# Kernel tuning notes

Measured on AMD Instinct MI355X. Metric: run time of the kernel, lower is better.

Reference implementation:

```python
import jax, jax.numpy as jnp
import numpy as np


def setup_inputs() -> dict:
    key = jax.random.key(0)
    k1, k2, k3, k4 = jax.random.split(key, 4)
    B, S, H, D = 4, 2048, 1024, 1024
    X = jax.random.normal(k1, (B, S, H), dtype=jnp.float32)
    # nn.Linear weight stored as [out, in]; we store as [in, out] for x @ W
    scale = 1.0 / np.sqrt(H)
    Wq = jax.random.normal(k2, (H, D), dtype=jnp.float32) * scale
    Wk = jax.random.normal(k3, (H, D), dtype=jnp.float32) * scale
    Wv = jax.random.normal(k4, (H, D), dtype=jnp.float32) * scale
    return {"X": X, "Wq": Wq, "Wk": Wk, "Wv": Wv}


def reference(X, Wq, Wk, Wv):
    B, S, H = X.shape
    q = X @ Wq  # [B, S, D]
    k = X @ Wk
    v = X @ Wv
    D = k.shape[-1]
    scores = jnp.einsum('bqd,bkd->bqk', q, k) / jnp.sqrt(jnp.float32(D))
    causal = jnp.tril(jnp.ones((S, S), dtype=bool))  # block_size mask sliced to S
    scores = jnp.where(causal, scores, -jnp.inf)
    weights = jax.nn.softmax(scores, axis=-1)  # dropout p=0.0 -> identity
    return jnp.einsum('bqk,bkd->bqd', weights, v)
```

## Files before the change

### kernel.cpp

```cpp
#include <hip/hip_runtime.h>

#define AS1 __attribute__((address_space(1)))
#define AS3 __attribute__((address_space(3)))

typedef __attribute__((ext_vector_type(8))) short short8;
typedef __attribute__((ext_vector_type(4))) float floatx4;

__device__ __forceinline__ short f2bf(float f) {
  union { float f; unsigned u; } v; v.f = f;
  return (short)((v.u + 0x7fffu + ((v.u >> 16) & 1u)) >> 16);
}
__device__ __forceinline__ float bf2f(short s) {
  union { unsigned u; float f; } v; v.u = ((unsigned)(unsigned short)s) << 16;
  return v.f;
}

__device__ __forceinline__ void gload_lds16(const void* g, void* l) {
  __builtin_amdgcn_global_load_lds((const AS1 unsigned*)g, (AS3 unsigned*)l, 16, 0, 0);
}

__device__ __forceinline__ void stage128x64(const short* __restrict__ G, long rowBase, long ld,
                                            int kBase, short* lds, int lane, int wave) {
  const int chunk = (lane & 7) ^ ((lane >> 3) & 7);
  const short* gb = G + rowBase * ld + (long)kBase + (long)(lane >> 3) * ld + chunk * 8;
#pragma unroll
  for (int j = 0; j < 4; ++j) {
    int c = wave * 4 + j;
    gload_lds16(gb + (long)c * 8 * ld, lds + c * 512);
  }
}

__device__ __forceinline__ void mfma_step(const short* lA, const short* lB, floatx4 acc[4][4],
                                          int lane, int wm, int wn) {
#pragma unroll
  for (int kk = 0; kk < 64; kk += 32) {
    short8 a[4], b[4];
    int kq = (kk + (lane >> 4) * 8) ^ ((lane & 7) << 3);
#pragma unroll
    for (int i = 0; i < 4; ++i) {
      a[i] = *(const short8*)(lA + (wm * 64 + i * 16 + (lane & 15)) * 64 + kq);
      b[i] = *(const short8*)(lB + (wn * 64 + i * 16 + (lane & 15)) * 64 + kq);
    }
#pragma unroll
    for (int i = 0; i < 4; ++i)
#pragma unroll
      for (int j = 0; j < 4; ++j)
        acc[i][j] = __builtin_amdgcn_mfma_f32_16x16x32_bf16(a[i], b[j], acc[i][j], 0, 0, 0);
  }
}

__device__ const unsigned char PAIR_LUT[136] = {
  0x40,0x41,0x42,0x43,0x50,0x51,0x52,0x53,0x60,0x61,0x62,0x63,0x70,0x71,0x72,0x73,
  0x80,0x81,0x82,0x83,0x90,0x91,0x92,0x93,0xA0,0xA1,0xA2,0xA3,0xB0,0xB1,0xB2,0xB3,
  0x84,0x85,0x86,0x87,0x94,0x95,0x96,0x97,0xA4,0xA5,0xA6,0xA7,0xB4,0xB5,0xB6,0xB7,
  0xC0,0xC1,0xC2,0xC3,0xD0,0xD1,0xD2,0xD3,0xE0,0xE1,0xE2,0xE3,0xF0,0xF1,0xF2,0xF3,
  0xC4,0xC5,0xC6,0xC7,0xD4,0xD5,0xD6,0xD7,0xE4,0xE5,0xE6,0xE7,0xF4,0xF5,0xF6,0xF7,
  0xC8,0xC9,0xCA,0xCB,0xD8,0xD9,0xDA,0xDB,0xE8,0xE9,0xEA,0xEB,0xF8,0xF9,0xFA,0xFB,
  0x00,0x10,0x11,0x20,0x21,0x22,0x30,0x31,0x32,0x33,
  0x44,0x54,0x55,0x64,0x65,0x66,0x74,0x75,0x76,0x77,
  0x88,0x98,0x99,0xA8,0xA9,0xAA,0xB8,0xB9,0xBA,0xBB,
  0xCC,0xDC,0xDD,0xEC,0xED,0xEE,0xFC,0xFD,0xFE,0xFF
};

__global__ void prep_inputs(const float* __restrict__ X, const float* __restrict__ Wq,
                            const float* __restrict__ Wk, const float* __restrict__ Wv,
                            short* __restrict__ Xb, short* __restrict__ Wt,
                            float* __restrict__ l) {
  __shared__ float t[32][33];
  if (blockIdx.x < 8192) {
    long i = ((long)blockIdx.x * 256 + threadIdx.x) * 4;
    float4 v = *(const float4*)(X + i);
    short4 o;
    o.x = f2bf(v.x); o.y = f2bf(v.y); o.z = f2bf(v.z); o.w = f2bf(v.w);
    *(short4*)(Xb + i) = o;
  } else if (blockIdx.x < 11264) {
    int idx = blockIdx.x - 8192;
    int z = idx >> 10, rem = idx & 1023;
    int bx = rem >> 5, by = rem & 31;
    const float* W = z == 0 ? Wq : (z == 1 ? Wk : Wv);
    short* O = Wt + (long)z * 1024 * 1024;
    int tx = threadIdx.x & 31, ty = threadIdx.x >> 5;
    int x = bx * 32 + tx;
    int y0 = by * 32;
    for (int j = ty; j < 32; j += 8)
      t[j][tx] = W[(long)(y0 + j) * 1024 + x];
    __syncthreads();
    int x2 = by * 32 + tx;
    int y2 = bx * 32;
    for (int j = ty; j < 32; j += 8)
      O[(long)(y2 + j) * 1024 + x2] = f2bf(t[tx][j]);
  } else {
    l[(blockIdx.x - 11264) * 256 + threadIdx.x] = 0.0f;
  }
}

#define LOFF(b, m, h) ((((b) * 2 + (m)) * 2 + (h)) * 8192)
#define MEMFENCE() asm volatile("" ::: "memory")
#define SBAR() do { MEMFENCE(); __builtin_amdgcn_s_barrier(); MEMFENCE(); } while (0)
#define SCHEDB() __builtin_amdgcn_sched_barrier(0)

__device__ __forceinline__ void stage_half(const short* __restrict__ g, short* l, int wv) {
  gload_lds16(g, l + wv * 512);
  gload_lds16(g + 65536, l + 4096 + wv * 512);
}

__device__ __forceinline__ short8 lds_rd(const short* l, int row, int kk, int lane) {
  const int r = row + (lane & 15);
  const int c = (kk + ((lane >> 4) << 3)) ^ ((lane & 7) << 3);
  return *(const short8*)(l + r * 64 + c);
}

__global__ __launch_bounds__(512, 2) void gemm_qkv(const short* __restrict__ Xb,
                                                   const short* __restrict__ Wt,
                                                   short* __restrict__ Q, short* __restrict__ K2,
                                                   short* __restrict__ Vt) {
  __shared__ __align__(16) short lds[65536];
  const int tid = threadIdx.x;
  const int lane = tid & 63, wv = tid >> 6;
  const int wm = wv >> 2, wn = wv & 3;

  const int bid = blockIdx.x;
  const int xcd = bid & 7, w = bid >> 3;
  const int mt = xcd * 4 + (w / 12);
  const int ng = w % 12;
  const int z = ng >> 2;
  const long mBase = (long)mt * 256;
  const long nBase = (long)(ng & 3) * 256;
  const short* Bm = Wt + (long)z * 1048576;

  const int r0 = tid >> 3;
  const int cc = ((tid & 7) ^ (r0 & 7)) << 3;
  const short* gA = Xb + (mBase + r0) * 1024 + cc;
  const short* gB = Bm + (nBase + r0) * 1024 + cc;

  floatx4 acc[8][4];
  const floatx4 zero = {0.f, 0.f, 0.f, 0.f};
#pragma unroll
  for (int i = 0; i < 8; ++i)
#pragma unroll
    for (int j = 0; j < 4; ++j) acc[i][j] = zero;

  short8 a0[4][2], a1[4][2], bq[2][2];

  stage_half(gA, lds + LOFF(0, 0, 0), wv);
  stage_half(gA + 131072, lds + LOFF(0, 0, 1), wv);
  stage_half(gB, lds + LOFF(0, 1, 0), wv);
  stage_half(gB + 131072, lds + LOFF(0, 1, 1), wv);
  stage_half(gA + 64, lds + LOFF(1, 0, 0), wv);
  stage_half(gA + 64 + 131072, lds + LOFF(1, 0, 1), wv);
  stage_half(gB + 64, lds + LOFF(1, 1, 0), wv);
  asm volatile("s_waitcnt vmcnt(6)" ::: "memory");
  SBAR();
  {
    const short* Ab0 = lds + LOFF(0, 0, wm);
#pragma unroll
    for (int f = 0; f < 4; ++f) a0[f][0] = lds_rd(Ab0, f * 16, 0, lane);
#pragma unroll
    for (int f = 0; f < 4; ++f) a0[f][1] = lds_rd(Ab0, f * 16, 32, lane);
  }

#pragma unroll 2
  for (int t = 0; t < 16; ++t) {
    const int buf = t & 1;
    const short* Ab  = lds + LOFF(buf, 0, wm);
    const short* Bb  = lds + LOFF(buf, 1, (wn >> 1));
    const short* AbN = lds + LOFF(buf ^ 1, 0, wm);
    const int brow = (wn & 1) * 64;

    bq[0][0] = lds_rd(Bb, brow, 0, lane);
    bq[1][0] = lds_rd(Bb, brow + 16, 0, lane);
    bq[0][1] = lds_rd(Bb, brow, 32, lane);
    bq[1][1] = lds_rd(Bb, brow + 16, 32, lane);
#pragma unroll
    for (int f = 0; f < 4; ++f) a1[f][0] = lds_rd(Ab, 64 + f * 16, 0, lane);
#pragma unroll
    for (int f = 0; f < 4; ++f) a1[f][1] = lds_rd(Ab, 64 + f * 16, 32, lane);
    if (t < 15) stage_half(gB + (t + 1) * 64 + 131072, lds + LOFF(buf ^ 1, 1, 1), wv);
    asm volatile("s_waitcnt lgkmcnt(8)" ::: "memory");
    SCHEDB();
    __builtin_amdgcn_s_setprio(1);
#pragma unroll
    for (int f = 0; f < 4; ++f)
#pragma unroll
      for (int n = 0; n < 2; ++n)
        acc[f][n] = __builtin_amdgcn_mfma_f32_16x16x32_bf16(a0[f][0], bq[n][0], acc[f][n], 0, 0, 0);
#pragma unroll
    for (int f = 0; f < 4; ++f)
#pragma unroll
      for (int n = 0; n < 2; ++n)
        acc[f][n] = __builtin_amdgcn_mfma_f32_16x16x32_bf16(a0[f][1], bq[n][1], acc[f][n], 0, 0, 0);
    __builtin_amdgcn_s_setprio(0);

    asm volatile("s_waitcnt lgkmcnt(0)" ::: "memory");
    SCHEDB();
    __builtin_amdgcn_s_setprio(1);
#pragma unroll
    for (int f = 0; f < 4; ++f)
#pragma unroll
      for (int n = 0; n < 2; ++n)
        acc[4 + f][n] = __builtin_amdgcn_mfma_f32_16x16x32_bf16(a1[f][0], bq[n][0], acc[4 + f][n], 0, 0, 0);
#pragma unroll
    for (int f = 0; f < 4; ++f)
#pragma unroll
      for (int n = 0; n < 2; ++n)
        acc[4 + f][n] = __builtin_amdgcn_mfma_f32_16x16x32_bf16(a1[f][1], bq[n][1], acc[4 + f][n], 0, 0, 0);
    __builtin_amdgcn_s_setprio(0);
    SBAR();

    bq[0][0] = lds_rd(Bb, brow + 32, 0, lane);
    bq[1][0] = lds_rd(Bb, brow + 48, 0, lane);
    bq[0][1] = lds_rd(Bb, brow + 32, 32, lane);
    bq[1][1] = lds_rd(Bb, brow + 48, 32, lane);
    if (t < 14) stage_half(gA + (t + 2) * 64, lds + LOFF(buf, 0, 0), wv);
    asm volatile("s_waitcnt lgkmcnt(0)" ::: "memory");
    SCHEDB();
    __builtin_amdgcn_s_setprio(1);
#pragma unroll
    for (int f = 0; f < 4; ++f)
#pragma unroll
      for (int n = 0; n < 2; ++n)
        acc[f][2 + n] = __builtin_amdgcn_mfma_f32_16x16x32_bf16(a0[f][0], bq[n][0], acc[f][2 + n], 0, 0, 0);
#pragma unroll
    for (int f = 0; f < 4; ++f)
#pragma unroll
      for (int n = 0; n < 2; ++n)
        acc[f][2 + n] = __builtin_amdgcn_mfma_f32_16x16x32_bf16(a0[f][1], bq[n][1], acc[f][2 + n], 0, 0, 0);
    __builtin_amdgcn_s_setprio(0);
    if (t < 14) { asm volatile("s_waitcnt vmcnt(2)" ::: "memory"); }
    else        { asm volatile("s_waitcnt vmcnt(0)" ::: "memory"); }
    SBAR();

    if (t < 15) {
#pragma unroll
      for (int f = 0; f < 4; ++f) a0[f][0] = lds_rd(AbN, f * 16, 0, lane);
#pragma unroll
      for (int f = 0; f < 4; ++f) a0[f][1] = lds_rd(AbN, f * 16, 32, lane);
    }
    if (t < 14) {
      stage_half(gA + (t + 2) * 64 + 131072, lds + LOFF(buf, 0, 1), wv);
      stage_half(gB + (t + 2) * 64, lds + LOFF(buf, 1, 0), wv);
    }
    SCHEDB();
    __builtin_amdgcn_s_setprio(1);
#pragma unroll
    for (int f = 0; f < 4; ++f)
#pragma unroll
      for (int n = 0; n < 2; ++n)
        acc[4 + f][2 + n] = __builtin_amdgcn_mfma_f32_16x16x32_bf16(a1[f][0], bq[n][0], acc[4 + f][2 + n], 0, 0, 0);
#pragma unroll
    for (int f = 0; f < 4; ++f)
#pragma unroll
      for (int n = 0; n < 2; ++n)
        acc[4 + f][2 + n] = __builtin_amdgcn_mfma_f32_16x16x32_bf16(a1[f][1], bq[n][1], acc[4 + f][2 + n], 0, 0, 0);
    __builtin_amdgcn_s_setprio(0);
  }

  if (z < 2) {
    short* outp = (z == 0) ? Q : K2;
#pragma unroll
    for (int f = 0; f < 8; ++f)
#pragma unroll
      for (int n = 0; n < 4; ++n) {
        const int col = (int)nBase + wn * 64 + n * 16 + (lane & 15);
#pragma unroll
        for (int rr = 0; rr < 4; ++rr) {
          const long m = mBase + wm * 128 + f * 16 + ((lane >> 4) << 2) + rr;
          outp[m * 1024 + col] = f2bf(acc[f][n][rr]);
        }
      }
  } else {
    const long bz = mBase >> 11;
    const int sB = (int)(mBase & 2047);
#pragma unroll
    for (int f = 0; f < 8; ++f) {
      const int s0 = sB + wm * 128 + f * 16 + ((lane >> 4) << 2);
#pragma unroll
      for (int n = 0; n < 4; ++n) {
        const int col = (int)nBase + wn * 64 + n * 16 + (lane & 15);
        short4 o;
        o.x = f2bf(acc[f][n][0]); o.y = f2bf(acc[f][n][1]);
        o.z = f2bf(acc[f][n][2]); o.w = f2bf(acc[f][n][3]);
        *(short4*)(Vt + ((bz * 1024 + col) * 2048 + s0)) = o;
      }
    }
  }
}

__global__ __launch_bounds__(256, 4) void scores_exp(const short* __restrict__ Q,
                                                     const short* __restrict__ Kk,
                                                     short* __restrict__ E, float* __restrict__ l) {
  __shared__ short lbuf[16384];
  short* lA = lbuf;
  short* lB = lbuf + 8192;
  const int lane = threadIdx.x & 63, wave = threadIdx.x >> 6;
  const int wm = wave >> 1, wn = wave & 1;
  const int b = blockIdx.y;

  const int r = blockIdx.x & 7, w = blockIdx.x >> 3;
  const int code = PAIR_LUT[r * 17 + w];
  const int qt = code >> 4, kt = code & 15;

  const long rowQ = (long)b * 2048 + (long)qt * 128;
  const long rowK = (long)b * 2048 + (long)kt * 128;

  floatx4 acc[4][4];
  const floatx4 zero = {0.f, 0.f, 0.f, 0.f};
#pragma unroll
  for (int i = 0; i < 4; ++i)
#pragma unroll
    for (int j = 0; j < 4; ++j) acc[i][j] = zero;

  for (int it = 0; it < 16; ++it) {
    stage128x64(Q, rowQ, 1024, it * 64, lA, lane, wave);
    stage128x64(Kk, rowK, 1024, it * 64, lB, lane, wave);
    __syncthreads();
    mfma_step(lA, lB, acc, lane, wm, wn);
    __syncthreads();
  }

  float* lrow = l + (long)b * 2048;
#pragma unroll
  for (int i = 0; i < 4; ++i) {
#pragma unroll
    for (int rr = 0; rr < 4; ++rr) {
      int ri = wm * 64 + i * 16 + (lane >> 4) * 4 + rr;
      int qrow = qt * 128 + ri;
      float psum = 0.f;
#pragma unroll
      for (int j = 0; j < 4; ++j) {
        int ci = wn * 64 + j * 16 + (lane & 15);
        int col = kt * 128 + ci;
        float sc = acc[i][j][rr] * 0.03125f;
        float e = (col <= qrow) ? __expf(sc) : 0.0f;
        short eb = f2bf(e);
        lbuf[ri * 128 + ((((ci >> 3) ^ (ri & 15)) << 3) | (ci & 7))] = eb;
        psum += bf2f(eb);
      }
      for (int m = 1; m < 16; m <<= 1) psum += __shfl_xor(psum, m, 64);
      if ((lane & 15) == 0) atomicAdd(&lrow[qrow], psum);
    }
  }
  __syncthreads();

  short* Eb = E + (long)b * 4194304;
  const long ebase = (long)(qt * 128) * 2048 + kt * 128;
#pragma unroll
  for (int pp = 0; pp < 8; ++pp) {
    int g = pp * 256 + threadIdx.x;
    int row = g >> 4, c = g & 15;
    short8 v = *(const short8*)(lbuf + row * 128 + ((c ^ (row & 15)) << 3));
    *(short8*)(Eb + ebase + (long)row * 2048 + c * 8) = v;
  }
}

__global__ __launch_bounds__(256, 4) void pv_gemm(const short* __restrict__ E,
                                                  const short* __restrict__ Vt,
                                                  const float* __restrict__ l,
                                                  float* __restrict__ part,
                                                  float* __restrict__ out) {
  __shared__ short lA[128 * 64], lB[128 * 64];
  const int lane = threadIdx.x & 63, wave = threadIdx.x >> 6;
  const int wm = wave >> 1, wn = wave & 1;
  const int xx = blockIdx.x;
  const int dt = xx / 24;
  const int within = xx % 24;
  const int r = within & 7, wsel = within >> 3;
  const int b = blockIdx.y;

  int qt, it0, it1, mode;
  if (wsel == 2) {
    qt = r; it0 = 0; it1 = (qt + 1) * 2; mode = 0;
  } else {
    qt = 15 - r;
    const int T = (qt + 1) * 2, c0 = T >> 1;
    if (wsel == 0) { it0 = 0;  it1 = c0; mode = 1; }
    else           { it0 = c0; it1 = T;  mode = 2; }
  }

  const short* Eb = E + (long)b * 2048 * 2048;
  const short* Vb = Vt + (long)b * 1024 * 2048;
  const float* lrow = l + (long)b * 2048;

  floatx4 acc[4][4];
  const floatx4 zero = {0.f, 0.f, 0.f, 0.f};
#pragma unroll
  for (int i = 0; i < 4; ++i)
#pragma unroll
    for (int j = 0; j < 4; ++j) acc[i][j] = zero;

  for (int it = it0; it < it1; ++it) {
    stage128x64(Eb, (long)qt * 128, 2048, it * 64, lA, lane, wave);
    stage128x64(Vb, (long)dt * 128, 2048, it * 64, lB, lane, wave);
    __syncthreads();
    mfma_step(lA, lB, acc, lane, wm, wn);
    __syncthreads();
  }

  if (mode == 2) {
    float* P = part + ((((long)b * 8 + (qt - 8)) * 8 + dt) << 14);
#pragma unroll
    for (int i = 0; i < 4; ++i)
#pragma unroll
      for (int rr = 0; rr < 4; ++rr) {
        int ri = wm * 64 + i * 16 + (lane >> 4) * 4 + rr;
#pragma unroll
        for (int j = 0; j < 4; ++j) {
          int ci = wn * 64 + j * 16 + (lane & 15);
          P[ri * 128 + ci] = acc[i][j][rr];
        }
      }
  } else {
#pragma unroll
    for (int i = 0; i < 4; ++i)
#pragma unroll
      for (int rr = 0; rr < 4; ++rr) {
        int qrow = qt * 128 + wm * 64 + i * 16 + (lane >> 4) * 4 + rr;
        float scale = (mode == 0) ? 1.0f / lrow[qrow] : 1.0f;
#pragma unroll
        for (int j = 0; j < 4; ++j) {
          int d = dt * 128 + wn * 64 + j * 16 + (lane & 15);
          out[((long)b * 2048 + qrow) * 1024 + d] = acc[i][j][rr] * scale;
        }
      }
  }
}

__global__ void pv_reduce(float* __restrict__ out, const float* __restrict__ part,
                          const float* __restrict__ l) {
  const int idx = blockIdx.x;
  const int b = idx >> 10;
  const int row = 1024 + (idx & 1023);
  const int t = threadIdx.x;
  const int dt = t >> 5, dl = (t << 2) & 127;
  const float inv = 1.0f / l[((long)b << 11) + row];
  const long pbase = ((((long)b * 8 + ((row >> 7) - 8)) * 8 + dt) << 14) + ((row & 127) << 7) + dl;
  const long obase = (((long)b * 2048 + row) << 10) + (t << 2);
  float4 o = *(const float4*)(out + obase);
  float4 p = *(const float4*)(part + pbase);
  o.x = (o.x + p.x) * inv; o.y = (o.y + p.y) * inv;
  o.z = (o.z + p.z) * inv; o.w = (o.w + p.w) * inv;
  *(float4*)(out + obase) = o;
}

extern "C" void kernel_launch(void* const* d_in, const int* in_sizes, int n_in,
                              void* d_out, int out_size, void* d_ws, size_t ws_size,
                              hipStream_t stream) {
  const float* X  = (const float*)d_in[0];
  const float* Wq = (const float*)d_in[1];
  const float* Wk = (const float*)d_in[2];
  const float* Wv = (const float*)d_in[3];

  char* ws = (char*)d_ws;
  short* Xb = (short*)(ws);
  short* Wt = (short*)(ws + 16777216L);
  short* Q  = (short*)(ws + 23068672L);
  short* K2 = (short*)(ws + 39845888L);
  short* Vt = (short*)(ws + 56623104L);
  short* E  = (short*)(ws + 73400320L);
  float* l  = (float*)(ws + 106954752L);
  float* part = (float*)(ws);

  prep_inputs<<<11296, 256, 0, stream>>>(X, Wq, Wk, Wv, Xb, Wt, l);
  gemm_qkv<<<384, 512, 0, stream>>>(Xb, Wt, Q, K2, Vt);
  scores_exp<<<dim3(136, 4), 256, 0, stream>>>(Q, K2, E, l);
  pv_gemm<<<dim3(192, 4), 256, 0, stream>>>(E, Vt, l, part, (float*)d_out);
  pv_reduce<<<4096, 256, 0, stream>>>((float*)d_out, part, l);
}
```

Baseline: 237.2 us.

## Double-buffer LDS staging in scores and PV GEMM kernels with async prefetch

Replaces the single-buffered load/sync/compute loops in scores_exp and pv_gemm with a two-stage LDS ring. The next K-tile is prefetched via global_load_lds while the current tile is consumed, with explicit vmcnt/lgkmcnt waits, sched barriers and setprio around the MFMA blocks. This aims to hide global memory latency behind the matrix math and to split LDS reads from MFMA issue. LDS per block doubles and launch bounds drop from 4 to 2 blocks per SM, which cuts occupancy.

```diff
diff --git a/kernel.cpp b/kernel.cpp
--- a/kernel.cpp
+++ b/kernel.cpp
@@ -30,24 +30,15 @@
   }
 }
 
-__device__ __forceinline__ void mfma_step(const short* lA, const short* lB, floatx4 acc[4][4],
-                                          int lane, int wm, int wn) {
-#pragma unroll
-  for (int kk = 0; kk < 64; kk += 32) {
-    short8 a[4], b[4];
-    int kq = (kk + (lane >> 4) * 8) ^ ((lane & 7) << 3);
-#pragma unroll
-    for (int i = 0; i < 4; ++i) {
-      a[i] = *(const short8*)(lA + (wm * 64 + i * 16 + (lane & 15)) * 64 + kq);
-      b[i] = *(const short8*)(lB + (wn * 64 + i * 16 + (lane & 15)) * 64 + kq);
-    }
-#pragma unroll
-    for (int i = 0; i < 4; ++i)
-#pragma unroll
-      for (int j = 0; j < 4; ++j)
-        acc[i][j] = __builtin_amdgcn_mfma_f32_16x16x32_bf16(a[i], b[j], acc[i][j], 0, 0, 0);
-  }
-}
+__device__ __forceinline__ short8 lds_rd(const short* l, int row, int kk, int lane) {
+  const int r = row + (lane & 15);
+  const int c = (kk + ((lane >> 4) << 3)) ^ ((lane & 7) << 3);
+  return *(const short8*)(l + r * 64 + c);
+}
+
+#define MEMFENCE() asm volatile("" ::: "memory")
+#define SBAR() do { MEMFENCE(); __builtin_amdgcn_s_barrier(); MEMFENCE(); } while (0)
+#define SCHEDB() __builtin_amdgcn_sched_barrier(0)
 
 __device__ const unsigned char PAIR_LUT[136] = {
   0x40,0x41,0x42,0x43,0x50,0x51,0x52,0x53,0x60,0x61,0x62,0x63,0x70,0x71,0x72,0x73,
@@ -95,19 +86,10 @@
 }
 
 #define LOFF(b, m, h) ((((b) * 2 + (m)) * 2 + (h)) * 8192)
-#define MEMFENCE() asm volatile("" ::: "memory")
-#define SBAR() do { MEMFENCE(); __builtin_amdgcn_s_barrier(); MEMFENCE(); } while (0)
-#define SCHEDB() __builtin_amdgcn_sched_barrier(0)
 
 __device__ __forceinline__ void stage_half(const short* __restrict__ g, short* l, int wv) {
   gload_lds16(g, l + wv * 512);
   gload_lds16(g + 65536, l + 4096 + wv * 512);
-}
-
-__device__ __forceinline__ short8 lds_rd(const short* l, int row, int kk, int lane) {
-  const int r = row + (lane & 15);
-  const int c = (kk + ((lane >> 4) << 3)) ^ ((lane & 7) << 3);
-  return *(const short8*)(l + r * 64 + c);
 }
 
 __global__ __launch_bounds__(512, 2) void gemm_qkv(const short* __restrict__ Xb,
@@ -286,12 +268,10 @@
   }
 }
 
-__global__ __launch_bounds__(256, 4) void scores_exp(const short* __restrict__ Q,
+__global__ __launch_bounds__(256, 2) void scores_exp(const short* __restrict__ Q,
                                                      const short* __restrict__ Kk,
                                                      short* __restrict__ E, float* __restrict__ l) {
-  __shared__ short lbuf[16384];
-  short* lA = lbuf;
-  short* lB = lbuf + 8192;
+  __shared__ __align__(16) short lds[32768];
   const int lane = threadIdx.x & 63, wave = threadIdx.x >> 6;
   const int wm = wave >> 1, wn = wave & 1;
   const int b = blockIdx.y;
@@ -310,14 +290,54 @@
 #pragma unroll
     for (int j = 0; j < 4; ++j) acc[i][j] = zero;
 
+  stage128x64(Q, rowQ, 1024, 0, lds, lane, wave);
+  stage128x64(Kk, rowK, 1024, 0, lds + 8192, lane, wave);
+  stage128x64(Q, rowQ, 1024, 64, lds + 16384, lane, wave);
+  stage128x64(Kk, rowK, 1024, 64, lds + 24576, lane, wave);
+  asm volatile("s_waitcnt vmcnt(8)" ::: "memory");
+  SBAR();
+
   for (int it = 0; it < 16; ++it) {
-    stage128x64(Q, rowQ, 1024, it * 64, lA, lane, wave);
-    stage128x64(Kk, rowK, 1024, it * 64, lB, lane, wave);
-    __syncthreads();
-    mfma_step(lA, lB, acc, lane, wm, wn);
-    __syncthreads();
-  }
-
+    const short* lA = lds + (it & 1) * 16384;
+    const short* lB = lA + 8192;
+    short8 a[4][2], bb[4][2];
+#pragma unroll
+    for (int i = 0; i < 4; ++i) a[i][0] = lds_rd(lA, wm * 64 + i * 16, 0, lane);
+#pragma unroll
+    for (int i = 0; i < 4; ++i) bb[i][0] = lds_rd(lB, wn * 64 + i * 16, 0, lane);
+#pragma unroll
+    for (int i = 0; i < 4; ++i) a[i][1] = lds_rd(lA, wm * 64 + i * 16, 32, lane);
+#pragma unroll
+    for (int i = 0; i < 4; ++i) bb[i][1] = lds_rd(lB, wn * 64 + i * 16, 32, lane);
+    asm volatile("s_waitcnt lgkmcnt(8)" ::: "memory");
+    SCHEDB();
+    __builtin_amdgcn_s_setprio(1);
+#pragma unroll
+    for (int i = 0; i < 4; ++i)
+#pragma unroll
+      for (int j = 0; j < 4; ++j)
+        acc[i][j] = __builtin_amdgcn_mfma_f32_16x16x32_bf16(a[i][0], bb[j][0], acc[i][j], 0, 0, 0);
+    asm volatile("s_waitcnt lgkmcnt(0)" ::: "memory");
+    SCHEDB();
+#pragma unroll
+    for (int i = 0; i < 4; ++i)
+#pragma unroll
+      for (int j = 0; j < 4; ++j)
+        acc[i][j] = __builtin_amdgcn_mfma_f32_16x16x32_bf16(a[i][1], bb[j][1], acc[i][j], 0, 0, 0);
+    __builtin_amdgcn_s_setprio(0);
+    SBAR();
+    if (it + 2 < 16) {
+      short* dst = lds + (it & 1) * 16384;
+      stage128x64(Q, rowQ, 1024, (it + 2) * 64, dst, lane, wave);
+      stage128x64(Kk, rowK, 1024, (it + 2) * 64, dst + 8192, lane, wave);
+      asm volatile("s_waitcnt vmcnt(8)" ::: "memory");
+    } else {
+      asm volatile("s_waitcnt vmcnt(0)" ::: "memory");
+    }
+    SBAR();
+  }
+
+  short* lbuf = lds;
   float* lrow = l + (long)b * 2048;
 #pragma unroll
   for (int i = 0; i < 4; ++i) {
@@ -353,12 +373,12 @@
   }
 }
 
-__global__ __launch_bounds__(256, 4) void pv_gemm(const short* __restrict__ E,
+__global__ __launch_bounds__(256, 2) void pv_gemm(const short* __restrict__ E,
                                                   const short* __restrict__ Vt,
                                                   const float* __restrict__ l,
                                                   float* __restrict__ part,
                                                   float* __restrict__ out) {
-  __shared__ short lA[128 * 64], lB[128 * 64];
+  __shared__ __align__(16) short lds[32768];
   const int lane = threadIdx.x & 63, wave = threadIdx.x >> 6;
   const int wm = wave >> 1, wn = wave & 1;
   const int xx = blockIdx.x;
@@ -380,6 +400,7 @@
   const short* Eb = E + (long)b * 2048 * 2048;
   const short* Vb = Vt + (long)b * 1024 * 2048;
   const float* lrow = l + (long)b * 2048;
+  const long rowE = (long)qt * 128, rowV = (long)dt * 128;
 
   floatx4 acc[4][4];
   const floatx4 zero = {0.f, 0.f, 0.f, 0.f};
@@ -388,12 +409,55 @@
 #pragma unroll
     for (int j = 0; j < 4; ++j) acc[i][j] = zero;
 
+  stage128x64(Eb, rowE, 2048, it0 * 64, lds, lane, wave);
+  stage128x64(Vb, rowV, 2048, it0 * 64, lds + 8192, lane, wave);
+  if (it0 + 1 < it1) {
+    stage128x64(Eb, rowE, 2048, (it0 + 1) * 64, lds + 16384, lane, wave);
+    stage128x64(Vb, rowV, 2048, (it0 + 1) * 64, lds + 24576, lane, wave);
+    asm volatile("s_waitcnt vmcnt(8)" ::: "memory");
+  } else {
+    asm volatile("s_waitcnt vmcnt(0)" ::: "memory");
+  }
+  SBAR();
+
   for (int it = it0; it < it1; ++it) {
-    stage128x64(Eb, (long)qt * 128, 2048, it * 64, lA, lane, wave);
-    stage128x64(Vb, (long)dt * 128, 2048, it * 64, lB, lane, wave);
-    __syncthreads();
-    mfma_step(lA, lB, acc, lane, wm, wn);
-    __syncthreads();
+    const short* lA = lds + ((it - it0) & 1) * 16384;
+    const short* lB = lA + 8192;
+    short8 a[4][2], bb[4][2];
+#pragma unroll
+    for (int i = 0; i < 4; ++i) a[i][0] = lds_rd(lA, wm * 64 + i * 16, 0, lane);
+#pragma unroll
+    for (int i = 0; i < 4; ++i) bb[i][0] = lds_rd(lB, wn * 64 + i * 16, 0, lane);
+#pragma unroll
+    for (int i = 0; i < 4; ++i) a[i][1] = lds_rd(lA, wm * 64 + i * 16, 32, lane);
+#pragma unroll
+    for (int i = 0; i < 4; ++i) bb[i][1] = lds_rd(lB, wn * 64 + i * 16, 32, lane);
+    asm volatile("s_waitcnt lgkmcnt(8)" ::: "memory");
+    SCHEDB();
+    __builtin_amdgcn_s_setprio(1);
+#pragma unroll
+    for (int i = 0; i < 4; ++i)
+#pragma unroll
+      for (int j = 0; j < 4; ++j)
+        acc[i][j] = __builtin_amdgcn_mfma_f32_16x16x32_bf16(a[i][0], bb[j][0], acc[i][j], 0, 0, 0);
+    asm volatile("s_waitcnt lgkmcnt(0)" ::: "memory");
+    SCHEDB();
+#pragma unroll
+    for (int i = 0; i < 4; ++i)
+#pragma unroll
+      for (int j = 0; j < 4; ++j)
+        acc[i][j] = __builtin_amdgcn_mfma_f32_16x16x32_bf16(a[i][1], bb[j][1], acc[i][j], 0, 0, 0);
+    __builtin_amdgcn_s_setprio(0);
+    SBAR();
+    if (it + 2 < it1) {
+      short* dst = lds + ((it - it0) & 1) * 16384;
+      stage128x64(Eb, rowE, 2048, (it + 2) * 64, dst, lane, wave);
+      stage128x64(Vb, rowV, 2048, (it + 2) * 64, dst + 8192, lane, wave);
+      asm volatile("s_waitcnt vmcnt(8)" ::: "memory");
+    } else {
+      asm volatile("s_waitcnt vmcnt(0)" ::: "memory");
+    }
+    SBAR();
   }
 
   if (mode == 2) {
```

Result: no change. 236.6 us (-0.3%).

## Widen scores and PV tiles to 128x256 so each block reuses its A tile

Applied to the files above, without the earlier changes.

Both scores_exp and pv_gemm now compute two adjacent 128-wide output tiles per block. Each block loads the shared Q or E tile once and keeps two accumulator sets, which cuts LDS staging and global traffic for the A operand. The grid sizes are halved to match: 72 blocks for scores with a new pair LUT, and 96 blocks for PV with an XCD-aware mapping. Occupancy drops from 4 to 2 blocks per CU because of the extra registers and LDS, and with far fewer blocks the GPU may be underfilled and load balance near the causal diagonal gets worse.

```diff
diff --git a/kernel.cpp b/kernel.cpp
--- a/kernel.cpp
+++ b/kernel.cpp
@@ -30,36 +30,33 @@
   }
 }
 
-__device__ __forceinline__ void mfma_step(const short* lA, const short* lB, floatx4 acc[4][4],
-                                          int lane, int wm, int wn) {
-#pragma unroll
-  for (int kk = 0; kk < 64; kk += 32) {
-    short8 a[4], b[4];
-    int kq = (kk + (lane >> 4) * 8) ^ ((lane & 7) << 3);
-#pragma unroll
-    for (int i = 0; i < 4; ++i) {
-      a[i] = *(const short8*)(lA + (wm * 64 + i * 16 + (lane & 15)) * 64 + kq);
-      b[i] = *(const short8*)(lB + (wn * 64 + i * 16 + (lane & 15)) * 64 + kq);
-    }
-#pragma unroll
-    for (int i = 0; i < 4; ++i)
-#pragma unroll
-      for (int j = 0; j < 4; ++j)
-        acc[i][j] = __builtin_amdgcn_mfma_f32_16x16x32_bf16(a[i], b[j], acc[i][j], 0, 0, 0);
-  }
-}
-
-__device__ const unsigned char PAIR_LUT[136] = {
-  0x40,0x41,0x42,0x43,0x50,0x51,0x52,0x53,0x60,0x61,0x62,0x63,0x70,0x71,0x72,0x73,
-  0x80,0x81,0x82,0x83,0x90,0x91,0x92,0x93,0xA0,0xA1,0xA2,0xA3,0xB0,0xB1,0xB2,0xB3,
-  0x84,0x85,0x86,0x87,0x94,0x95,0x96,0x97,0xA4,0xA5,0xA6,0xA7,0xB4,0xB5,0xB6,0xB7,
-  0xC0,0xC1,0xC2,0xC3,0xD0,0xD1,0xD2,0xD3,0xE0,0xE1,0xE2,0xE3,0xF0,0xF1,0xF2,0xF3,
-  0xC4,0xC5,0xC6,0xC7,0xD4,0xD5,0xD6,0xD7,0xE4,0xE5,0xE6,0xE7,0xF4,0xF5,0xF6,0xF7,
-  0xC8,0xC9,0xCA,0xCB,0xD8,0xD9,0xDA,0xDB,0xE8,0xE9,0xEA,0xEB,0xF8,0xF9,0xFA,0xFB,
-  0x00,0x10,0x11,0x20,0x21,0x22,0x30,0x31,0x32,0x33,
-  0x44,0x54,0x55,0x64,0x65,0x66,0x74,0x75,0x76,0x77,
-  0x88,0x98,0x99,0xA8,0xA9,0xAA,0xB8,0xB9,0xBA,0xBB,
-  0xCC,0xDC,0xDD,0xEC,0xED,0xEE,0xFC,0xFD,0xFE,0xFF
+__device__ __forceinline__ short8 lds_rd(const short* l, int row, int kk, int lane) {
+  const int r = row + (lane & 15);
+  const int c = (kk + ((lane >> 4) << 3)) ^ ((lane & 7) << 3);
+  return *(const short8*)(l + r * 64 + c);
+}
+
+#define MEMFENCE() asm volatile("" ::: "memory")
+#define SBAR() do { MEMFENCE(); __builtin_amdgcn_s_barrier(); MEMFENCE(); } while (0)
+#define SCHEDB() __builtin_amdgcn_sched_barrier(0)
+
+__device__ const unsigned char PAIR72[72] = {
+  0x00,
+  0x10,
+  0x20,0x21,
+  0x30,0x31,
+  0x40,0x41,0x42,
+  0x50,0x51,0x52,
+  0x60,0x61,0x62,0x63,
+  0x70,0x71,0x72,0x73,
+  0x80,0x81,0x82,0x83,0x84,
+  0x90,0x91,0x92,0x93,0x94,
+  0xA0,0xA1,0xA2,0xA3,0xA4,0xA5,
+  0xB0,0xB1,0xB2,0xB3,0xB4,0xB5,
+  0xC0,0xC1,0xC2,0xC3,0xC4,0xC5,0xC6,
+  0xD0,0xD1,0xD2,0xD3,0xD4,0xD5,0xD6,
+  0xE0,0xE1,0xE2,0xE3,0xE4,0xE5,0xE6,0xE7,
+  0xF0,0xF1,0xF2,0xF3,0xF4,0xF5,0xF6,0xF7
 };
 
 __global__ void prep_inputs(const float* __restrict__ X, const float* __restrict__ Wq,
@@ -95,19 +92,10 @@
 }
 
 #define LOFF(b, m, h) ((((b) * 2 + (m)) * 2 + (h)) * 8192)
-#define MEMFENCE() asm volatile("" ::: "memory")
-#define SBAR() do { MEMFENCE(); __builtin_amdgcn_s_barrier(); MEMFENCE(); } while (0)
-#define SCHEDB() __builtin_amdgcn_sched_barrier(0)
 
 __device__ __forceinline__ void stage_half(const short* __restrict__ g, short* l, int wv) {
   gload_lds16(g, l + wv * 512);
   gload_lds16(g + 65536, l + 4096 + wv * 512);
-}
-
-__device__ __forceinline__ short8 lds_rd(const short* l, int row, int kk, int lane) {
-  const int r = row + (lane & 15);
-  const int c = (kk + ((lane >> 4) << 3)) ^ ((lane & 7) << 3);
-  return *(const short8*)(l + r * 64 + c);
 }
 
 __global__ __launch_bounds__(512, 2) void gemm_qkv(const short* __restrict__ Xb,
@@ -286,84 +274,131 @@
   }
 }
 
-__global__ __launch_bounds__(256, 4) void scores_exp(const short* __restrict__ Q,
+__global__ __launch_bounds__(256, 2) void scores_exp(const short* __restrict__ Q,
                                                      const short* __restrict__ Kk,
                                                      short* __restrict__ E, float* __restrict__ l) {
-  __shared__ short lbuf[16384];
-  short* lA = lbuf;
-  short* lB = lbuf + 8192;
+  __shared__ __align__(16) short lds[24576];
+  short* lQ = lds;
+  short* lK0 = lds + 8192;
+  short* lK1 = lds + 16384;
   const int lane = threadIdx.x & 63, wave = threadIdx.x >> 6;
   const int wm = wave >> 1, wn = wave & 1;
   const int b = blockIdx.y;
 
-  const int r = blockIdx.x & 7, w = blockIdx.x >> 3;
-  const int code = PAIR_LUT[r * 17 + w];
-  const int qt = code >> 4, kt = code & 15;
+  const int cls = blockIdx.x & 7, idx = blockIdx.x >> 3;
+  const int code = PAIR72[cls * 9 + idx];
+  const int qt = code >> 4, ktp = code & 15;
+  const int kt0 = ktp * 2, kt1 = kt0 + 1;
+  const bool two = (kt1 <= qt);
 
   const long rowQ = (long)b * 2048 + (long)qt * 128;
-  const long rowK = (long)b * 2048 + (long)kt * 128;
-
-  floatx4 acc[4][4];
+  const long rowK0 = (long)b * 2048 + (long)kt0 * 128;
+  const long rowK1 = rowK0 + 128;
+
+  floatx4 acc0[4][4], acc1[4][4];
   const floatx4 zero = {0.f, 0.f, 0.f, 0.f};
 #pragma unroll
   for (int i = 0; i < 4; ++i)
 #pragma unroll
-    for (int j = 0; j < 4; ++j) acc[i][j] = zero;
+    for (int j = 0; j < 4; ++j) { acc0[i][j] = zero; acc1[i][j] = zero; }
 
   for (int it = 0; it < 16; ++it) {
-    stage128x64(Q, rowQ, 1024, it * 64, lA, lane, wave);
-    stage128x64(Kk, rowK, 1024, it * 64, lB, lane, wave);
+    stage128x64(Q, rowQ, 1024, it * 64, lQ, lane, wave);
+    stage128x64(Kk, rowK0, 1024, it * 64, lK0, lane, wave);
+    if (two) stage128x64(Kk, rowK1, 1024, it * 64, lK1, lane, wave);
     __syncthreads();
-    mfma_step(lA, lB, acc, lane, wm, wn);
+    short8 a[4][2], bb[4][2];
+#pragma unroll
+    for (int i = 0; i < 4; ++i) {
+      a[i][0] = lds_rd(lQ, wm * 64 + i * 16, 0, lane);
+      a[i][1] = lds_rd(lQ, wm * 64 + i * 16, 32, lane);
+    }
+#pragma unroll
+    for (int i = 0; i < 4; ++i) {
+      bb[i][0] = lds_rd(lK0, wn * 64 + i * 16, 0, lane);
+      bb[i][1] = lds_rd(lK0, wn * 64 + i * 16, 32, lane);
+    }
+#pragma unroll
+    for (int ks = 0; ks < 2; ++ks)
+#pragma unroll
+      for (int i = 0; i < 4; ++i)
+#pragma unroll
+        for (int j = 0; j < 4; ++j)
+          acc0[i][j] = __builtin_amdgcn_mfma_f32_16x16x32_bf16(a[i][ks], bb[j][ks], acc0[i][j], 0, 0, 0);
+    if (two) {
+#pragma unroll
+      for (int i = 0; i < 4; ++i) {
+        bb[i][0] = lds_rd(lK1, wn * 64 + i * 16, 0, lane);
+        bb[i][1] = lds_rd(lK1, wn * 64 + i * 16, 32, lane);
+      }
+#pragma unroll
+      for (int ks = 0; ks < 2; ++ks)
+#pragma unroll
+        for (int i = 0; i < 4; ++i)
+#pragma unroll
+          for (int j = 0; j < 4; ++j)
+            acc1[i][j] = __builtin_amdgcn_mfma_f32_16x16x32_bf16(a[i][ks], bb[j][ks], acc1[i][j], 0, 0, 0);
+    }
     __syncthreads();
   }
 
+  short* lbuf = lds;
   float* lrow = l + (long)b * 2048;
-#pragma unroll
-  for (int i = 0; i < 4; ++i) {
-#pragma unroll
-    for (int rr = 0; rr < 4; ++rr) {
-      int ri = wm * 64 + i * 16 + (lane >> 4) * 4 + rr;
-      int qrow = qt * 128 + ri;
-      float psum = 0.f;
-#pragma unroll
-      for (int j = 0; j < 4; ++j) {
-        int ci = wn * 64 + j * 16 + (lane & 15);
-        int col = kt * 128 + ci;
-        float sc = acc[i][j][rr] * 0.03125f;
-        float e = (col <= qrow) ? __expf(sc) : 0.0f;
-        short eb = f2bf(e);
-        lbuf[ri * 128 + ((((ci >> 3) ^ (ri & 15)) << 3) | (ci & 7))] = eb;
-        psum += bf2f(eb);
+  short* Eb = E + (long)b * 4194304;
+#pragma unroll 1
+  for (int tsel = 0; tsel < 2; ++tsel) {
+    if (tsel == 1 && !two) break;
+    const int kt = tsel == 0 ? kt0 : kt1;
+    floatx4 (&acc)[4][4] = tsel == 0 ? acc0 : acc1;
+    if (tsel == 1) __syncthreads();
+#pragma unroll
+    for (int i = 0; i < 4; ++i) {
+#pragma unroll
+      for (int rr = 0; rr < 4; ++rr) {
+        int ri = wm * 64 + i * 16 + (lane >> 4) * 4 + rr;
+        int qrow = qt * 128 + ri;
+        float psum = 0.f;
+#pragma unroll
+        for (int j = 0; j < 4; ++j) {
+          int ci = wn * 64 + j * 16 + (lane & 15);
+          int col = kt * 128 + ci;
+          float sc = acc[i][j][rr] * 0.03125f;
+          float e = (col <= qrow) ? __expf(sc) : 0.0f;
+          short eb = f2bf(e);
+          lbuf[ri * 128 + ((((ci >> 3) ^ (ri & 15)) << 3) | (ci & 7))] = eb;
+          psum += bf2f(eb);
+        }
+        for (int m = 1; m < 16; m <<= 1) psum += __shfl_xor(psum, m, 64);
+        if ((lane & 15) == 0) atomicAdd(&lrow[qrow], psum);
       }
-      for (int m = 1; m < 16; m <<= 1) psum += __shfl_xor(psum, m, 64);
-      if ((lane & 15) == 0) atomicAdd(&lrow[qrow], psum);
-    }
-  }
-  __syncthreads();
-
-  short* Eb = E + (long)b * 4194304;
-  const long ebase = (long)(qt * 128) * 2048 + kt * 128;
-#pragma unroll
-  for (int pp = 0; pp < 8; ++pp) {
-    int g = pp * 256 + threadIdx.x;
-    int row = g >> 4, c = g & 15;
-    short8 v = *(const short8*)(lbuf + row * 128 + ((c ^ (row & 15)) << 3));
-    *(short8*)(Eb + ebase + (long)row * 2048 + c * 8) = v;
-  }
-}
-
-__global__ __launch_bounds__(256, 4) void pv_gemm(const short* __restrict__ E,
+    }
+    __syncthreads();
+    const long ebase = (long)(qt * 128) * 2048 + kt * 128;
+#pragma unroll
+    for (int pp = 0; pp < 8; ++pp) {
+      int g = pp * 256 + threadIdx.x;
+      int row = g >> 4, c = g & 15;
+      short8 v = *(const short8*)(lbuf + row * 128 + ((c ^ (row & 15)) << 3));
+      *(short8*)(Eb + ebase + (long)row * 2048 + c * 8) = v;
+    }
+  }
+}
+
+__global__ __launch_bounds__(256, 2) void pv_gemm(const short* __restrict__ E,
                                                   const short* __restrict__ Vt,
                                                   const float* __restrict__ l,
                                                   float* __restrict__ part,
                                                   float* __restrict__ out) {
-  __shared__ short lA[128 * 64], lB[128 * 64];
+  __shared__ __align__(16) short lds[24576];
+  short* lE = lds;
+  short* lV0 = lds + 8192;
+  short* lV1 = lds + 16384;
   const int lane = threadIdx.x & 63, wave = threadIdx.x >> 6;
   const int wm = wave >> 1, wn = wave & 1;
-  const int xx = blockIdx.x;
-  const int dt = xx / 24;
-  const int within = xx % 24;
+  const int x = blockIdx.x;
+  const int xcd = x & 7, w = x >> 3;
+  const int dt0 = xcd >> 1, dt1 = dt0 + 4;
+  const int within = (xcd & 1) * 12 + w;
   const int r = within & 7, wsel = within >> 3;
   const int b = blockIdx.y;
 
@@ -380,24 +415,57 @@
   const short* Eb = E + (long)b * 2048 * 2048;
   const short* Vb = Vt + (long)b * 1024 * 2048;
   const float* lrow = l + (long)b * 2048;
-
-  floatx4 acc[4][4];
+  const long rowE = (long)qt * 128;
+  const long rowV0 = (long)dt0 * 128, rowV1 = (long)dt1 * 128;
+
+  floatx4 acc0[4][4], acc1[4][4];
   const floatx4 zero = {0.f, 0.f, 0.f, 0.f};
 #pragma unroll
   for (int i = 0; i < 4; ++i)
 #pragma unroll
-    for (int j = 0; j < 4; ++j) acc[i][j] = zero;
+    for (int j = 0; j < 4; ++j) { acc0[i][j] = zero; acc1[i][j] = zero; }
 
   for (int it = it0; it < it1; ++it) {
-    stage128x64(Eb, (long)qt * 128, 2048, it * 64, lA, lane, wave);
-    stage128x64(Vb, (long)dt * 128, 2048, it * 64, lB, lane, wave);
+    stage128x64(Eb, rowE, 2048, it * 64, lE, lane, wave);
+    stage128x64(Vb, rowV0, 2048, it * 64, lV0, lane, wave);
+    stage128x64(Vb, rowV1, 2048, it * 64, lV1, lane, wave);
     __syncthreads();
-    mfma_step(lA, lB, acc, lane, wm, wn);
+    short8 a[4][2], bb[4][2];
+#pragma unroll
+    for (int i = 0; i < 4; ++i) {
+      a[i][0] = lds_rd(lE, wm * 64 + i * 16, 0, lane);
+      a[i][1] = lds_rd(lE, wm * 64 + i * 16, 32, lane);
+    }
+#pragma unroll
+    for (int i = 0; i < 4; ++i) {
+      bb[i][0] = lds_rd(lV0, wn * 64 + i * 16, 0, lane);
+      bb[i][1] = lds_rd(lV0, wn * 64 + i * 16, 32, lane);
+    }
+#pragma unroll
+    for (int ks = 0; ks < 2; ++ks)
+#pragma unroll
+      for (int i = 0; i < 4; ++i)
+#pragma unroll
+        for (int j = 0; j < 4; ++j)
+          acc0[i][j] = __builtin_amdgcn_mfma_f32_16x16x32_bf16(a[i][ks], bb[j][ks], acc0[i][j], 0, 0, 0);
+#pragma unroll
+    for (int i = 0; i < 4; ++i) {
+      bb[i][0] = lds_rd(lV1, wn * 64 + i * 16, 0, lane);
+      bb[i][1] = lds_rd(lV1, wn * 64 + i * 16, 32, lane);
+    }
+#pragma unroll
+    for (int ks = 0; ks < 2; ++ks)
+#pragma unroll
+      for (int i = 0; i < 4; ++i)
+#pragma unroll
+        for (int j = 0; j < 4; ++j)
+          acc1[i][j] = __builtin_amdgcn_mfma_f32_16x16x32_bf16(a[i][ks], bb[j][ks], acc1[i][j], 0, 0, 0);
     __syncthreads();
   }
 
   if (mode == 2) {
-    float* P = part + ((((long)b * 8 + (qt - 8)) * 8 + dt) << 14);
+    float* P0 = part + ((((long)b * 8 + (qt - 8)) * 8 + dt0) << 14);
+    float* P1 = part + ((((long)b * 8 + (qt - 8)) * 8 + dt1) << 14);
 #pragma unroll
     for (int i = 0; i < 4; ++i)
 #pragma unroll
@@ -406,7 +474,8 @@
 #pragma unroll
         for (int j = 0; j < 4; ++j) {
           int ci = wn * 64 + j * 16 + (lane & 15);
-          P[ri * 128 + ci] = acc[i][j][rr];
+          P0[ri * 128 + ci] = acc0[i][j][rr];
+          P1[ri * 128 + ci] = acc1[i][j][rr];
         }
       }
   } else {
@@ -418,8 +487,9 @@
         float scale = (mode == 0) ? 1.0f / lrow[qrow] : 1.0f;
 #pragma unroll
         for (int j = 0; j < 4; ++j) {
-          int d = dt * 128 + wn * 64 + j * 16 + (lane & 15);
-          out[((long)b * 2048 + qrow) * 1024 + d] = acc[i][j][rr] * scale;
+          int ci = wn * 64 + j * 16 + (lane & 15);
+          out[((long)b * 2048 + qrow) * 1024 + dt0 * 128 + ci] = acc0[i][j][rr] * scale;
+          out[((long)b * 2048 + qrow) * 1024 + dt1 * 128 + ci] = acc1[i][j][rr] * scale;
         }
       }
   }
@@ -462,7 +532,7 @@
 
   prep_inputs<<<11296, 256, 0, stream>>>(X, Wq, Wk, Wv, Xb, Wt, l);
   gemm_qkv<<<384, 512, 0, stream>>>(Xb, Wt, Q, K2, Vt);
-  scores_exp<<<dim3(136, 4), 256, 0, stream>>>(Q, K2, E, l);
-  pv_gemm<<<dim3(192, 4), 256, 0, stream>>>(E, Vt, l, part, (float*)d_out);
+  scores_exp<<<dim3(72, 4), 256, 0, stream>>>(Q, K2, E, l);
+  pv_gemm<<<dim3(96, 4), 256, 0, stream>>>(E, Vt, l, part, (float*)d_out);
   pv_reduce<<<4096, 256, 0, stream>>>((float*)d_out, part, l);
 }
```

Measured after the change: 230.9 us, median of 2. 2.7% less time.
